# Kernel tuning notes

Hardware: AMD Instinct MI355X
Metric: run time of the kernel (lower is better)

Reference implementation:

```python
import jax, jax.numpy as jnp
import numpy as np

BATCH = 1
SEQ = 3072
HID = 1024
HEADS = 16
HDIM = HID // HEADS  # 64
NSEQ = 8
SLEN = 380
ROPE_BASE = 10.0


def _boundaries():
    b, start = [], 0
    for _ in range(NSEQ):
        b.append((start, start + SLEN))
        start = start + SLEN + 1  # +1 for SEP token
    return b


def setup_inputs() -> dict:
    key = jax.random.key(0)
    ks = jax.random.split(key, 10)
    bnd = _boundaries()
    L = bnd[-1][1]  # actual_length = 3047
    # block-diagonal mask; SEP tokens attend only to themselves
    mask = np.zeros((L, L), dtype=bool)
    for s, e in bnd:
        mask[s:e, s:e] = True
    for s, e in bnd[:-1]:
        mask[e, e] = True
    # position ids reset at each sequence start
    pos = np.zeros((SEQ,), dtype=np.int32)
    for s, e in bnd:
        pos[s:e] = np.arange(e - s, dtype=np.int32)
    sc = 1.0 / np.sqrt(HID)
    return {
        "x": jax.random.normal(ks[0], (BATCH, SEQ, HID), jnp.float32),
        "wq": jax.random.normal(ks[1], (HID, HID), jnp.float32) * sc,
        "bq": jnp.zeros((HID,), jnp.float32),
        "wk": jax.random.normal(ks[2], (HID, HID), jnp.float32) * sc,
        "bk": jnp.zeros((HID,), jnp.float32),
        "wv": jax.random.normal(ks[3], (HID, HID), jnp.float32) * sc,
        "bv": jnp.zeros((HID,), jnp.float32),
        "wo": jax.random.normal(ks[4], (HID, HID), jnp.float32) * sc,
        "bo": jnp.zeros((HID,), jnp.float32),
        "mask": jnp.asarray(mask),
        "position_ids": jnp.asarray(pos)[None, :],  # [1, SEQ]
    }


def _apply_rope(q, k, pos):
    # q, k: [B, S, H, D]; pos: [B, S]
    half = HDIM // 2
    inv_freq = 1.0 / (ROPE_BASE ** (jnp.arange(0, HDIM, 2, dtype=jnp.float32) / HDIM))
    ang = pos.astype(jnp.float32)[..., None] * inv_freq  # [B, S, half]
    cos = jnp.cos(ang)[:, :, None, :]  # [B, S, 1, half]
    sin = jnp.sin(ang)[:, :, None, :]

    def rot(t):
        t1, t2 = t[..., :half], t[..., half:]
        return jnp.concatenate([t1 * cos - t2 * sin, t1 * sin + t2 * cos], axis=-1)

    return rot(q), rot(k)


def reference(x, wq, bq, wk, bk, wv, bv, wo, bo, mask, position_ids):
    B, S, _ = x.shape
    L = mask.shape[0]  # actual_length (static)
    q = (x @ wq.T + bq).reshape(B, S, HEADS, HDIM)
    k = (x @ wk.T + bk).reshape(B, S, HEADS, HDIM)
    v = (x @ wv.T + bv).reshape(B, S, HEADS, HDIM)
    q, k = _apply_rope(q, k, position_ids)
    # [B, H, S, D], trim to packed length
    q = q.transpose(0, 2, 1, 3)[:, :, :L, :]
    k = k.transpose(0, 2, 1, 3)[:, :, :L, :]
    v = v.transpose(0, 2, 1, 3)[:, :, :L, :]
    scores = jnp.einsum("bhqd,bhkd->bhqk", q, k) / jnp.sqrt(jnp.float32(HDIM))
    scores = jnp.where(mask[None, None], scores, -jnp.inf)
    attn = jax.nn.softmax(scores, axis=-1)
    out = jnp.einsum("bhqk,bhkd->bhqd", attn, v)  # [B, H, L, D]
    out = jnp.pad(out, ((0, 0), (0, 0), (0, S - L), (0, 0)))  # zero padded tail
    out = out.transpose(0, 2, 1, 3).reshape(B, S, HID)
    return out @ wo.T + bo
```

## Files before the change

### kernel.cpp

```cpp
#include <hip/hip_runtime.h>

typedef unsigned short u16;
typedef __attribute__((ext_vector_type(8))) short short8;
typedef __attribute__((ext_vector_type(4))) float f32x4;

#define SEQ 3072
#define HID 1024
#define HEADS 16
#define HDIM 64
#define SEGLEN 380
#define SEGSTR 381
#define NSEG 8
#define LTOT 3047
#define VPAD 384

static __device__ __forceinline__ u16 f2bf(float f) {
  unsigned u = __builtin_bit_cast(unsigned, f);
  u += 0x7fffu + ((u >> 16) & 1u);
  return (u16)(u >> 16);
}
static __device__ __forceinline__ float bf2f(u16 h) {
  unsigned u = ((unsigned)h) << 16;
  return __builtin_bit_cast(float, u);
}

static __device__ __forceinline__ void load_lds16(const void* g, void* l) {
  __builtin_amdgcn_global_load_lds((const __attribute__((address_space(1))) void*)g,
                                   (__attribute__((address_space(3))) void*)l, 16, 0, 0);
}

#define BAR() __builtin_amdgcn_s_barrier()
#define VM(N) asm volatile("s_waitcnt vmcnt(" #N ")" ::: "memory")

__global__ void cvt_all_kernel(const float* __restrict__ x, const float* __restrict__ wq,
                               const float* __restrict__ wk, const float* __restrict__ wv,
                               const float* __restrict__ wo, u16* __restrict__ out) {
  const int i = blockIdx.x * 256 + threadIdx.x;
  const float* s;
  int base;
  if (i < 786432)       { s = x;  base = 0; }
  else if (i < 1048576) { s = wq; base = 786432; }
  else if (i < 1310720) { s = wk; base = 1048576; }
  else if (i < 1572864) { s = wv; base = 1310720; }
  else                  { s = wo; base = 1572864; }
  float4 v = reinterpret_cast<const float4*>(s)[i - base];
  unsigned long long o = (unsigned long long)f2bf(v.x) |
                         ((unsigned long long)f2bf(v.y) << 16) |
                         ((unsigned long long)f2bf(v.z) << 32) |
                         ((unsigned long long)f2bf(v.w) << 48);
  reinterpret_cast<unsigned long long*>(out)[i] = o;
}

static __device__ __forceinline__ void stage_qkv(
    const u16* __restrict__ A, const u16* __restrict__ Bw,
    u16* As, u16* Bs, int rowBase, int colBase, int k0) {
  const int tid = threadIdx.x;
  const int w = tid >> 6;
  const int row = tid >> 2;
  const int j = (tid & 3) ^ ((row >> 1) & 3);
  load_lds16(A + (size_t)(rowBase + row) * HID + k0 + j * 8, As + (w * 64) * 8);
  load_lds16(Bw + (size_t)(colBase + row) * HID + k0 + j * 8, Bs + (w * 64) * 8);
}

static __device__ __forceinline__ void compute_qkv(
    const u16* As, const u16* Bs, int wr, int cb0, int lc, int lh, f32x4 (*acc)[2]) {
  short8 af[4], bfv[2];
#pragma unroll
  for (int m = 0; m < 4; ++m) {
    const int row = wr + m * 16 + lc;
    af[m] = *reinterpret_cast<const short8*>(As + row * 32 + (lh ^ ((row >> 1) & 3)) * 8);
  }
#pragma unroll
  for (int n = 0; n < 2; ++n) {
    const int row = cb0 + n * 32 + lc;
    bfv[n] = *reinterpret_cast<const short8*>(Bs + row * 32 + (lh ^ ((row >> 1) & 3)) * 8);
  }
  __builtin_amdgcn_s_setprio(1);
#pragma unroll
  for (int m = 0; m < 4; ++m)
#pragma unroll
    for (int n = 0; n < 2; ++n)
      acc[m][n] = __builtin_amdgcn_mfma_f32_16x16x32_bf16(af[m], bfv[n], acc[m][n], 0, 0, 0);
  __builtin_amdgcn_s_setprio(0);
}

__global__ __launch_bounds__(512) void qkv_gemm_kernel(
    const u16* __restrict__ xb,
    const u16* __restrict__ wqb, const u16* __restrict__ wkb, const u16* __restrict__ wvb,
    const float* __restrict__ bq, const float* __restrict__ bk, const float* __restrict__ bv,
    u16* __restrict__ qb, u16* __restrict__ kbuf, u16* __restrict__ vT) {
  __shared__ u16 As[3][128 * 32];
  __shared__ u16 Bs[3][128 * 32];
  const int which = blockIdx.y >> 3;
  const u16* Bw = (which == 0) ? wqb : (which == 1) ? wkb : wvb;
  const float* bias = (which == 0) ? bq : (which == 1) ? bk : bv;
  const int rowBase = blockIdx.x * 128;
  const int colBase = (blockIdx.y & 7) * 128;
  const int tid = threadIdx.x;
  const int w = tid >> 6, l = tid & 63, lc = l & 15, lh = l >> 4;
  const int wr = (w >> 2) * 64;
  const int c2 = w & 3;
  const int cb0 = (c2 >> 1) * 64 + (c2 & 1) * 16;

  f32x4 acc[4][2];
  f32x4 z4 = {0.f, 0.f, 0.f, 0.f};
#pragma unroll
  for (int m = 0; m < 4; ++m) { acc[m][0] = z4; acc[m][1] = z4; }

  stage_qkv(xb, Bw, As[0], Bs[0], rowBase, colBase, 0);
  stage_qkv(xb, Bw, As[1], Bs[1], rowBase, colBase, 32);
#pragma unroll 1
  for (int t = 0; t < 30; t += 3) {
    stage_qkv(xb, Bw, As[2], Bs[2], rowBase, colBase, (t + 2) * 32);
    VM(4); BAR();
    compute_qkv(As[0], Bs[0], wr, cb0, lc, lh, acc);
    BAR();
    stage_qkv(xb, Bw, As[0], Bs[0], rowBase, colBase, (t + 3) * 32);
    VM(4); BAR();
    compute_qkv(As[1], Bs[1], wr, cb0, lc, lh, acc);
    BAR();
    stage_qkv(xb, Bw, As[1], Bs[1], rowBase, colBase, (t + 4) * 32);
    VM(4); BAR();
    compute_qkv(As[2], Bs[2], wr, cb0, lc, lh, acc);
    BAR();
  }
  VM(2); BAR();
  compute_qkv(As[0], Bs[0], wr, cb0, lc, lh, acc);
  BAR();
  VM(0); BAR();
  compute_qkv(As[1], Bs[1], wr, cb0, lc, lh, acc);

  const int f = (c2 & 1) * 16 + lc;
  const int col0 = colBase + (c2 >> 1) * 64 + f;
  if (which < 2) {
    u16* outp = which ? kbuf : qb;
    const float bv0 = bias[col0];
    const float bv1 = bias[col0 + 32];
    const float invf = exp2f(-(float)f * 0.10381025296523007f);
#pragma unroll
    for (int m = 0; m < 4; ++m) {
      const int row0 = rowBase + wr + m * 16 + lh * 4;
#pragma unroll
      for (int r = 0; r < 4; ++r) {
        const int row = row0 + r;
        const int rr = row % SEGSTR;
        const float pos = (float)((rr < SEGLEN) ? rr : 0);
        float sn, cs;
        sincosf(pos * invf, &sn, &cs);
        const float t1 = acc[m][0][r] + bv0;
        const float t2 = acc[m][1][r] + bv1;
        const size_t base = (size_t)row * HID + col0;
        outp[base] = f2bf(t1 * cs - t2 * sn);
        outp[base + 32] = f2bf(t1 * sn + t2 * cs);
      }
    }
  } else {
#pragma unroll
    for (int n = 0; n < 2; ++n) {
      const int col = col0 + n * 32;
      const float bvl = bias[col];
#pragma unroll
      for (int m = 0; m < 4; ++m) {
        const int row0 = rowBase + wr + m * 16 + lh * 4;
#pragma unroll
        for (int r = 0; r < 4; ++r) {
          const float v = acc[m][n][r] + bvl;
          const int row = row0 + r;
          const int sg = row / SEGSTR;
          const int j = row - sg * SEGSTR;
          if (sg < NSEG)
            vT[(size_t)col * (NSEG * VPAD) + sg * VPAD + j] = f2bf(v);
        }
      }
    }
  }
}

static __device__ __forceinline__ void stage_out(
    const u16* __restrict__ A, const u16* __restrict__ Bw,
    u16* As, u16* Bs, int rowBase, int colBase, int k0) {
  const int tid = threadIdx.x;
  const int w = tid >> 6;
#pragma unroll
  for (int c = 0; c < 2; ++c) {
    const int li = c * 512 + tid;
    const int row = li >> 3;
    const int j = (li & 7) ^ (row & 7);
    load_lds16(A + (size_t)(rowBase + row) * HID + k0 + j * 8,
               As + (c * 512 + w * 64) * 8);
  }
  {
    const int row = tid >> 3;
    const int j = (tid & 7) ^ (row & 7);
    load_lds16(Bw + (size_t)(colBase + row) * HID + k0 + j * 8, Bs + (w * 64) * 8);
  }
}

static __device__ __forceinline__ void compute_out(
    const u16* As, const u16* Bs, int wrO, int wcO, int lc, int lh, f32x4 (*acc)[2]) {
  short8 af[2][2], bfv[2][2];
#pragma unroll
  for (int m = 0; m < 2; ++m) {
    const int row = wrO + m * 16 + lc;
#pragma unroll
    for (int ks = 0; ks < 2; ++ks)
      af[m][ks] = *reinterpret_cast<const short8*>(
          As + row * 64 + (((ks * 4 + lh) ^ (row & 7))) * 8);
  }
#pragma unroll
  for (int n = 0; n < 2; ++n) {
    const int row = wcO + n * 16 + lc;
#pragma unroll
    for (int ks = 0; ks < 2; ++ks)
      bfv[n][ks] = *reinterpret_cast<const short8*>(
          Bs + row * 64 + (((ks * 4 + lh) ^ (row & 7))) * 8);
  }
  __builtin_amdgcn_s_setprio(1);
#pragma unroll
  for (int ks = 0; ks < 2; ++ks)
#pragma unroll
    for (int m = 0; m < 2; ++m)
#pragma unroll
      for (int n = 0; n < 2; ++n)
        acc[m][n] = __builtin_amdgcn_mfma_f32_16x16x32_bf16(af[m][ks], bfv[n][ks], acc[m][n], 0, 0, 0);
  __builtin_amdgcn_s_setprio(0);
}

__global__ __launch_bounds__(512) void out_gemm_kernel(
    const u16* __restrict__ aob, const u16* __restrict__ wob,
    const float* __restrict__ bo, float* __restrict__ out) {
  __shared__ u16 As[3][128 * 64];
  __shared__ u16 Bs[3][64 * 64];
  const int rowBase = blockIdx.x * 128;
  const int colBase = blockIdx.y * 64;
  const int tid = threadIdx.x;
  const int w = tid >> 6, l = tid & 63, lc = l & 15, lh = l >> 4;
  const int wrO = (w >> 1) * 32, wcO = (w & 1) * 32;
  f32x4 acc[2][2];
  f32x4 z4 = {0.f, 0.f, 0.f, 0.f};
#pragma unroll
  for (int m = 0; m < 2; ++m) { acc[m][0] = z4; acc[m][1] = z4; }

  stage_out(aob, wob, As[0], Bs[0], rowBase, colBase, 0);
  stage_out(aob, wob, As[1], Bs[1], rowBase, colBase, 64);
#pragma unroll 1
  for (int t = 0; t < 12; t += 3) {
    stage_out(aob, wob, As[2], Bs[2], rowBase, colBase, (t + 2) * 64);
    VM(6); BAR();
    compute_out(As[0], Bs[0], wrO, wcO, lc, lh, acc);
    BAR();
    stage_out(aob, wob, As[0], Bs[0], rowBase, colBase, (t + 3) * 64);
    VM(6); BAR();
    compute_out(As[1], Bs[1], wrO, wcO, lc, lh, acc);
    BAR();
    stage_out(aob, wob, As[1], Bs[1], rowBase, colBase, (t + 4) * 64);
    VM(6); BAR();
    compute_out(As[2], Bs[2], wrO, wcO, lc, lh, acc);
    BAR();
  }
  stage_out(aob, wob, As[2], Bs[2], rowBase, colBase, 14 * 64);
  VM(6); BAR();
  compute_out(As[0], Bs[0], wrO, wcO, lc, lh, acc);
  BAR();
  stage_out(aob, wob, As[0], Bs[0], rowBase, colBase, 15 * 64);
  VM(6); BAR();
  compute_out(As[1], Bs[1], wrO, wcO, lc, lh, acc);
  BAR();
  VM(3); BAR();
  compute_out(As[2], Bs[2], wrO, wcO, lc, lh, acc);
  BAR();
  VM(0); BAR();
  compute_out(As[0], Bs[0], wrO, wcO, lc, lh, acc);

#pragma unroll
  for (int n = 0; n < 2; ++n) {
    const int col = colBase + wcO + n * 16 + lc;
    const float bvl = bo[col];
#pragma unroll
    for (int m = 0; m < 2; ++m) {
      const int row0 = rowBase + wrO + m * 16 + lh * 4;
#pragma unroll
      for (int r = 0; r < 4; ++r)
        out[(size_t)(row0 + r) * HID + col] = acc[m][n][r] + bvl;
    }
  }
}

__global__ __launch_bounds__(256) void attn_kernel(
    const u16* __restrict__ qb, const u16* __restrict__ kb,
    const u16* __restrict__ vT, u16* __restrict__ ao) {
  __shared__ u16 Ks[3][32 * 64];
  __shared__ u16 Vs[3][64 * 32];
  __shared__ u16 P_lds[4][16 * 32];
  const int tid = threadIdx.x;
  const int w = tid >> 6, l = tid & 63, lc = l & 15, lh = l >> 4;
  const int W = (blockIdx.x & 7) * 96 + (blockIdx.x >> 3);
  const int qt = W % 6;
  const int seg = (W / 6) & 7;
  const int h = W / 48;
  const int segbase = seg * SEGSTR;
  const int rloc = qt * 64 + w * 16;

  const u16* qrow = qb + (size_t)(segbase + rloc + lc) * HID + h * HDIM + lh * 8;
  const short8 qf0 = *reinterpret_cast<const short8*>(qrow);
  const short8 qf1 = *reinterpret_cast<const short8*>(qrow + 32);

  const size_t vstride = (size_t)NSEG * VPAD;
  const u16* kseg = kb + (size_t)segbase * HID + h * HDIM;
  const u16* vseg = vT + (size_t)h * HDIM * vstride + seg * VPAD;

  const int krow = tid >> 3;
  const int kj = (tid & 7) ^ (krow & 7);
  const int vd = tid >> 2;
  const int vj = (tid & 3) ^ ((vd >> 2) & 3);

  f32x4 z4 = {0.f, 0.f, 0.f, 0.f};
  f32x4 accO[4] = {z4, z4, z4, z4};
  float psum[4] = {0.f, 0.f, 0.f, 0.f};

  u16* pl = &P_lds[w][0];
  int wo0[4], wo1[4];
#pragma unroll
  for (int r = 0; r < 4; ++r) {
    const int prow = lh * 4 + r;
    const int sw = (prow >> 1) & 3;
    wo0[r] = prow * 32 + ((lc >> 3) ^ sw) * 8 + (lc & 7);
    wo1[r] = prow * 32 + ((2 + (lc >> 3)) ^ sw) * 8 + (lc & 7);
  }
  const int prd_off = lc * 32 + (lh ^ ((lc >> 1) & 3)) * 8;

#define STAGE(B, T)                                                                 \
  load_lds16(kseg + (size_t)((T) * 32 + krow) * HID + kj * 8, &Ks[B][0] + w * 512); \
  load_lds16(vseg + (size_t)vd * vstride + (T) * 32 + vj * 8, &Vs[B][0] + w * 512);

#define STEP(B, MASKED)                                                               \
  {                                                                                   \
    const u16* KB = &Ks[B][0];                                                        \
    const u16* VB = &Vs[B][0];                                                        \
    const int ks0 = (lh ^ (lc & 7)) * 8;                                              \
    const int ks1 = ((lh + 4) ^ (lc & 7)) * 8;                                        \
    const short8 k00 = *reinterpret_cast<const short8*>(KB + lc * 64 + ks0);          \
    const short8 k01 = *reinterpret_cast<const short8*>(KB + lc * 64 + ks1);          \
    const short8 k10 = *reinterpret_cast<const short8*>(KB + (16 + lc) * 64 + ks0);   \
    const short8 k11 = *reinterpret_cast<const short8*>(KB + (16 + lc) * 64 + ks1);   \
    f32x4 s0 = z4, s1 = z4;                                                           \
    __builtin_amdgcn_s_setprio(1);                                                    \
    s0 = __builtin_amdgcn_mfma_f32_16x16x32_bf16(qf0, k00, s0, 0, 0, 0);              \
    s0 = __builtin_amdgcn_mfma_f32_16x16x32_bf16(qf1, k01, s0, 0, 0, 0);              \
    s1 = __builtin_amdgcn_mfma_f32_16x16x32_bf16(qf0, k10, s1, 0, 0, 0);              \
    s1 = __builtin_amdgcn_mfma_f32_16x16x32_bf16(qf1, k11, s1, 0, 0, 0);              \
    __builtin_amdgcn_s_setprio(0);                                                    \
    float p0[4], p1[4];                                                               \
    _Pragma("unroll") for (int r = 0; r < 4; ++r) {                                   \
      p0[r] = (!(MASKED) || lc < 28) ? __expf(s0[r] * 0.125f) : 0.f;                  \
      p1[r] = (!(MASKED) || lc < 12) ? __expf(s1[r] * 0.125f) : 0.f;                  \
      psum[r] += p0[r] + p1[r];                                                       \
    }                                                                                 \
    _Pragma("unroll") for (int r = 0; r < 4; ++r) {                                   \
      pl[wo0[r]] = f2bf(p0[r]);                                                       \
      pl[wo1[r]] = f2bf(p1[r]);                                                       \
    }                                                                                 \
    const short8 pf = *reinterpret_cast<const short8*>(pl + prd_off);                 \
    const int vsw = (lh ^ (lc >> 2)) * 8;                                             \
    const short8 v0 = *reinterpret_cast<const short8*>(VB + lc * 32 + vsw);           \
    const short8 v1 = *reinterpret_cast<const short8*>(VB + (16 + lc) * 32 + vsw);    \
    const short8 v2 = *reinterpret_cast<const short8*>(VB + (32 + lc) * 32 + vsw);    \
    const short8 v3 = *reinterpret_cast<const short8*>(VB + (48 + lc) * 32 + vsw);    \
    __builtin_amdgcn_s_setprio(1);                                                    \
    accO[0] = __builtin_amdgcn_mfma_f32_16x16x32_bf16(pf, v0, accO[0], 0, 0, 0);      \
    accO[1] = __builtin_amdgcn_mfma_f32_16x16x32_bf16(pf, v1, accO[1], 0, 0, 0);      \
    accO[2] = __builtin_amdgcn_mfma_f32_16x16x32_bf16(pf, v2, accO[2], 0, 0, 0);      \
    accO[3] = __builtin_amdgcn_mfma_f32_16x16x32_bf16(pf, v3, accO[3], 0, 0, 0);      \
    __builtin_amdgcn_s_setprio(0);                                                    \
  }

  STAGE(0, 0);
  STAGE(1, 1);
#pragma unroll 1
  for (int t = 0; t < 9; t += 3) {
    STAGE(2, t + 2);
    VM(4); BAR();
    STEP(0, false);
    BAR();
    STAGE(0, t + 3);
    VM(4); BAR();
    STEP(1, false);
    BAR();
    STAGE(1, t + 4);
    VM(4); BAR();
    STEP(2, false);
    BAR();
  }
  STAGE(2, 11);
  VM(4); BAR();
  STEP(0, false);
  BAR();
  VM(2); BAR();
  STEP(1, false);
  BAR();
  VM(0); BAR();
  STEP(2, true);
#undef STEP
#undef STAGE

  float inv[4];
#pragma unroll
  for (int r = 0; r < 4; ++r) {
    float s = psum[r];
    s += __shfl_xor(s, 1);
    s += __shfl_xor(s, 2);
    s += __shfl_xor(s, 4);
    s += __shfl_xor(s, 8);
    inv[r] = 1.0f / s;
  }
#pragma unroll
  for (int r = 0; r < 4; ++r) {
    const int lrow = rloc + lh * 4 + r;
    if (lrow < SEGLEN) {
      const size_t orow = (size_t)(segbase + lrow) * HID + h * HDIM;
#pragma unroll
      for (int n = 0; n < 4; ++n)
        ao[orow + n * 16 + lc] = f2bf(accO[n][r] * inv[r]);
    }
  }
}

__global__ void fixup_kernel(const u16* __restrict__ vT, u16* __restrict__ ao) {
  int idx = blockIdx.x * 256 + threadIdx.x;
  int r = idx >> 10, c = idx & 1023;
  if (r < NSEG - 1) {
    int row = r * SEGSTR + SEGLEN;
    ao[(size_t)row * HID + c] = vT[(size_t)c * (NSEG * VPAD) + r * VPAD + SEGLEN];
  } else {
    int row = LTOT + (r - (NSEG - 1));
    ao[(size_t)row * HID + c] = 0;
  }
}

extern "C" void kernel_launch(void* const* d_in, const int* in_sizes, int n_in,
                              void* d_out, int out_size, void* d_ws, size_t ws_size,
                              hipStream_t stream) {
  const float* x  = (const float*)d_in[0];
  const float* wq = (const float*)d_in[1];
  const float* bq = (const float*)d_in[2];
  const float* wk = (const float*)d_in[3];
  const float* bk = (const float*)d_in[4];
  const float* wv = (const float*)d_in[5];
  const float* bv = (const float*)d_in[6];
  const float* wo = (const float*)d_in[7];
  const float* bo = (const float*)d_in[8];
  float* out = (float*)d_out;

  u16* ws = (u16*)d_ws;
  u16* xb   = ws;
  u16* wqb  = xb  + (size_t)SEQ * HID;
  u16* wkb  = wqb + (size_t)HID * HID;
  u16* wvb  = wkb + (size_t)HID * HID;
  u16* wob  = wvb + (size_t)HID * HID;
  u16* qb   = wob + (size_t)HID * HID;
  u16* kbuf = qb  + (size_t)SEQ * HID;
  u16* vT   = kbuf + (size_t)SEQ * HID;
  u16* aob  = vT  + (size_t)HID * (NSEG * VPAD);

  cvt_all_kernel<<<7168, 256, 0, stream>>>(x, wq, wk, wv, wo, ws);

  qkv_gemm_kernel<<<dim3(SEQ / 128, 24), 512, 0, stream>>>(
      xb, wqb, wkb, wvb, bq, bk, bv, qb, kbuf, vT);

  attn_kernel<<<768, 256, 0, stream>>>(qb, kbuf, vT, aob);

  fixup_kernel<<<32 * 1024 / 256, 256, 0, stream>>>(vT, aob);

  out_gemm_kernel<<<dim3(SEQ / 128, HID / 64), 512, 0, stream>>>(aob, wob, bo, out);

  (void)in_sizes; (void)n_in; (void)out_size; (void)ws_size;
}
```

Baseline: 80.78 us.

## Widen QKV GEMM K-tile to 64 with double buffering and fold fixup into attention

The QKV GEMM K-step grows from 32 to 64. The LDS goes from triple to double buffering, with an 8-way XOR swizzle, and each compute stage issues two MFMA k-substeps. This halves the barrier and loop count per output tile. Separately, the SEP-token copy and zero-padding fixup kernel is removed and its work is done inside the attention kernel by the qt==5 blocks, which saves one launch. The trade-off is a shallower prefetch pipeline, and the VM(4) wait counts may need re-checking now that each thread issues four loads per stage.

```diff
diff --git a/kernel.cpp b/kernel.cpp
--- a/kernel.cpp
+++ b/kernel.cpp
@@ -56,31 +56,43 @@
     u16* As, u16* Bs, int rowBase, int colBase, int k0) {
   const int tid = threadIdx.x;
   const int w = tid >> 6;
-  const int row = tid >> 2;
-  const int j = (tid & 3) ^ ((row >> 1) & 3);
-  load_lds16(A + (size_t)(rowBase + row) * HID + k0 + j * 8, As + (w * 64) * 8);
-  load_lds16(Bw + (size_t)(colBase + row) * HID + k0 + j * 8, Bs + (w * 64) * 8);
+#pragma unroll
+  for (int c = 0; c < 2; ++c) {
+    const int li = c * 512 + tid;
+    const int row = li >> 3;
+    const int j = (li & 7) ^ (row & 7);
+    load_lds16(A + (size_t)(rowBase + row) * HID + k0 + j * 8, As + (c * 512 + w * 64) * 8);
+    load_lds16(Bw + (size_t)(colBase + row) * HID + k0 + j * 8, Bs + (c * 512 + w * 64) * 8);
+  }
 }
 
 static __device__ __forceinline__ void compute_qkv(
     const u16* As, const u16* Bs, int wr, int cb0, int lc, int lh, f32x4 (*acc)[2]) {
-  short8 af[4], bfv[2];
+  short8 af[4][2], bfv[2][2];
 #pragma unroll
   for (int m = 0; m < 4; ++m) {
     const int row = wr + m * 16 + lc;
-    af[m] = *reinterpret_cast<const short8*>(As + row * 32 + (lh ^ ((row >> 1) & 3)) * 8);
+#pragma unroll
+    for (int ks = 0; ks < 2; ++ks)
+      af[m][ks] = *reinterpret_cast<const short8*>(
+          As + row * 64 + (((ks * 4 + lh) ^ (row & 7))) * 8);
   }
 #pragma unroll
   for (int n = 0; n < 2; ++n) {
     const int row = cb0 + n * 32 + lc;
-    bfv[n] = *reinterpret_cast<const short8*>(Bs + row * 32 + (lh ^ ((row >> 1) & 3)) * 8);
+#pragma unroll
+    for (int ks = 0; ks < 2; ++ks)
+      bfv[n][ks] = *reinterpret_cast<const short8*>(
+          Bs + row * 64 + (((ks * 4 + lh) ^ (row & 7))) * 8);
   }
   __builtin_amdgcn_s_setprio(1);
 #pragma unroll
-  for (int m = 0; m < 4; ++m)
-#pragma unroll
-    for (int n = 0; n < 2; ++n)
-      acc[m][n] = __builtin_amdgcn_mfma_f32_16x16x32_bf16(af[m], bfv[n], acc[m][n], 0, 0, 0);
+  for (int ks = 0; ks < 2; ++ks)
+#pragma unroll
+    for (int m = 0; m < 4; ++m)
+#pragma unroll
+      for (int n = 0; n < 2; ++n)
+        acc[m][n] = __builtin_amdgcn_mfma_f32_16x16x32_bf16(af[m][ks], bfv[n][ks], acc[m][n], 0, 0, 0);
   __builtin_amdgcn_s_setprio(0);
 }
 
@@ -89,8 +101,8 @@
     const u16* __restrict__ wqb, const u16* __restrict__ wkb, const u16* __restrict__ wvb,
     const float* __restrict__ bq, const float* __restrict__ bk, const float* __restrict__ bv,
     u16* __restrict__ qb, u16* __restrict__ kbuf, u16* __restrict__ vT) {
-  __shared__ u16 As[3][128 * 32];
-  __shared__ u16 Bs[3][128 * 32];
+  __shared__ u16 As[2][128 * 64];
+  __shared__ u16 Bs[2][128 * 64];
   const int which = blockIdx.y >> 3;
   const u16* Bw = (which == 0) ? wqb : (which == 1) ? wkb : wvb;
   const float* bias = (which == 0) ? bq : (which == 1) ? bk : bv;
@@ -108,23 +120,19 @@
   for (int m = 0; m < 4; ++m) { acc[m][0] = z4; acc[m][1] = z4; }
 
   stage_qkv(xb, Bw, As[0], Bs[0], rowBase, colBase, 0);
-  stage_qkv(xb, Bw, As[1], Bs[1], rowBase, colBase, 32);
 #pragma unroll 1
-  for (int t = 0; t < 30; t += 3) {
-    stage_qkv(xb, Bw, As[2], Bs[2], rowBase, colBase, (t + 2) * 32);
+  for (int t = 0; t < 14; t += 2) {
+    stage_qkv(xb, Bw, As[1], Bs[1], rowBase, colBase, (t + 1) * 64);
     VM(4); BAR();
     compute_qkv(As[0], Bs[0], wr, cb0, lc, lh, acc);
     BAR();
-    stage_qkv(xb, Bw, As[0], Bs[0], rowBase, colBase, (t + 3) * 32);
+    stage_qkv(xb, Bw, As[0], Bs[0], rowBase, colBase, (t + 2) * 64);
     VM(4); BAR();
     compute_qkv(As[1], Bs[1], wr, cb0, lc, lh, acc);
     BAR();
-    stage_qkv(xb, Bw, As[1], Bs[1], rowBase, colBase, (t + 4) * 32);
-    VM(4); BAR();
-    compute_qkv(As[2], Bs[2], wr, cb0, lc, lh, acc);
-    BAR();
-  }
-  VM(2); BAR();
+  }
+  stage_qkv(xb, Bw, As[1], Bs[1], rowBase, colBase, 15 * 64);
+  VM(4); BAR();
   compute_qkv(As[0], Bs[0], wr, cb0, lc, lh, acc);
   BAR();
   VM(0); BAR();
@@ -423,17 +431,22 @@
         ao[orow + n * 16 + lc] = f2bf(accO[n][r] * inv[r]);
     }
   }
-}
-
-__global__ void fixup_kernel(const u16* __restrict__ vT, u16* __restrict__ ao) {
-  int idx = blockIdx.x * 256 + threadIdx.x;
-  int r = idx >> 10, c = idx & 1023;
-  if (r < NSEG - 1) {
-    int row = r * SEGSTR + SEGLEN;
-    ao[(size_t)row * HID + c] = vT[(size_t)c * (NSEG * VPAD) + r * VPAD + SEGLEN];
-  } else {
-    int row = LTOT + (r - (NSEG - 1));
-    ao[(size_t)row * HID + c] = 0;
+
+  if (qt == 5) {
+    if (seg < NSEG - 1) {
+      if (tid < HDIM)
+        ao[(size_t)(segbase + SEGLEN) * HID + h * HDIM + tid] =
+            vT[(size_t)(h * HDIM + tid) * vstride + seg * VPAD + SEGLEN];
+    } else {
+#pragma unroll
+      for (int k = 0; k < 7; ++k) {
+        const int idx = k * 256 + tid;
+        if (idx < 25 * HDIM) {
+          const int rr = idx >> 6, cc = idx & 63;
+          ao[(size_t)(LTOT + rr) * HID + h * HDIM + cc] = 0;
+        }
+      }
+    }
   }
 }
 
@@ -469,8 +482,6 @@
 
   attn_kernel<<<768, 256, 0, stream>>>(qb, kbuf, vT, aob);
 
-  fixup_kernel<<<32 * 1024 / 256, 256, 0, stream>>>(vT, aob);
-
   out_gemm_kernel<<<dim3(SEQ / 128, HID / 64), 512, 0, stream>>>(aob, wob, bo, out);
 
   (void)in_sizes; (void)n_in; (void)out_size; (void)ws_size;
```

Result: no change. 80.29 us (-0.6%).
